# Optimization experiments

Hardware: AMD Instinct MI355X
Metric: run time of the kernel (lower is better)

## Reference

```python
import jax, jax.numpy as jnp
import numpy as np

GRID, BOXN, LABELN = 14, 2, 20
COORD_RATE, NOOBJ_RATE = 5.0, 0.5
CELL = 1.0 / GRID  # cell_size = 1/grid_num
ALL_BOX = 5 * BOXN


def setup_inputs() -> dict:
    key = jax.random.key(0)
    k1, k2, k3 = jax.random.split(key, 3)
    B = 4096
    C = ALL_BOX + LABELN  # 30
    preds = jax.random.uniform(k1, (B, GRID, GRID, C), dtype=jnp.float32)
    truths = jax.random.uniform(k2, (B, GRID, GRID, C), dtype=jnp.float32)
    objm = jax.random.uniform(k3, (B, GRID, GRID)) < 0.08
    truths = truths.at[..., 4].set(jnp.where(objm, truths[..., 4], 0.0))
    return {"preds": preds, "truths": truths}


def _yolo_loss(preds, truths):
    B = preds.shape[0]
    dt = preds.dtype
    obj = truths[..., 4] > 0                                   # [B,S,S]
    pb = preds[..., :ALL_BOX].reshape(*preds.shape[:3], BOXN, 5)  # [B,S,S,Bx,5]
    tb = truths[..., 0:4]                                       # [B,S,S,4]

    # ---- IoU of every predicted box vs the truth box of its cell ----
    pc = CELL * pb[..., 0:2]; ph = pb[..., 2:4] / 2.0
    tc = CELL * tb[..., 0:2]; th = tb[..., 2:4] / 2.0
    p_lt, p_rb = pc - ph, pc + ph                               # [B,S,S,Bx,2]
    t_lt, t_rb = (tc - th)[..., None, :], (tc + th)[..., None, :]  # [B,S,S,1,2]
    lt = jnp.maximum(p_lt, t_lt)
    rb = jnp.minimum(p_rb, t_rb)
    wh = jnp.clip(rb - lt, 0.0, None)
    inter = wh[..., 0] * wh[..., 1]                             # [B,S,S,Bx]
    pa = (p_rb[..., 0] - p_lt[..., 0]) * (p_rb[..., 1] - p_lt[..., 1])
    ta = (t_rb[..., 0] - t_lt[..., 0]) * (t_rb[..., 1] - t_lt[..., 1])
    ious = inter / (pa + ta - inter)                            # [B,S,S,Bx]

    # ---- responsible-box selection (argmax IoU; ties broken by max conf) ----
    max_iou = jnp.max(ious, axis=-1)                            # [B,S,S]
    tied = ious == max_iou[..., None]
    n_tied = tied.sum(-1)
    conf = pb[..., 4]                                           # [B,S,S,Bx]
    ind_conf = jnp.argmax(jnp.where(tied, conf, -jnp.inf), axis=-1)
    ind_iou = jnp.argmax(ious, axis=-1)
    resp = jnp.where(n_tied > 1, ind_conf, ind_iou)             # [B,S,S]
    resp_oh = jax.nn.one_hot(resp, BOXN, dtype=bool)            # [B,S,S,Bx]

    w_obj = obj.astype(dt)
    pred_resp = jnp.take_along_axis(pb, resp[..., None, None], axis=3)[..., 0, :]  # [B,S,S,5]
    tbox5 = truths[..., 0:5]

    center_loss = jnp.sum(w_obj[..., None] * (pred_resp[..., 0:2] - tbox5[..., 0:2]) ** 2)
    size_loss = jnp.sum(w_obj[..., None] * (jnp.sqrt(pred_resp[..., 2:4]) - jnp.sqrt(tbox5[..., 2:4])) ** 2)
    t_conf = jax.lax.stop_gradient(max_iou)  # .item() in torch detaches the IoU target
    conf_resp_loss = jnp.sum(w_obj * (pred_resp[..., 4] - t_conf) ** 2)
    noresp = (obj[..., None] & (~resp_oh)).astype(dt)
    conf_noresp_loss = jnp.sum(noresp * conf ** 2)
    conf_noobj_loss = jnp.sum((~obj)[..., None].astype(dt) * conf ** 2)
    label_loss = jnp.sum(w_obj[..., None] * (preds[..., ALL_BOX:] - truths[..., ALL_BOX:]) ** 2)

    return (COORD_RATE * (center_loss + size_loss) + conf_resp_loss
            + NOOBJ_RATE * conf_noresp_loss + NOOBJ_RATE * conf_noobj_loss
            + label_loss) / B


def reference(preds, truths):
    return _yolo_loss(preds, truths)
```

## Files before the change

kernel.cpp:

```cpp
#include <hip/hip_runtime.h>
#include <math.h>

#define GRIDN   14
#define BOXN    2
#define LABELN  20
#define ALL_BOX 10
#define CCH     30
#define CELLS_PER_BLOCK 256

__global__ void yolo_zero_kernel(float* out, int n) {
    int i = blockIdx.x * blockDim.x + threadIdx.x;
    if (i < n) out[i] = 0.0f;
}

__device__ __forceinline__ void async_load16(const float* g, float* l) {
    __builtin_amdgcn_global_load_lds(
        (const __attribute__((address_space(1))) void*)g,
        (__attribute__((address_space(3))) void*)l,
        16, 0, 0);
}

__global__ __launch_bounds__(256) void yolo_loss_kernel(
    const float* __restrict__ preds,
    const float* __restrict__ truths,
    float* __restrict__ out,
    int ncells)
{
#pragma clang fp contract(off)
    __shared__ float sP[CELLS_PER_BLOCK * CCH];
    __shared__ float sT[CELLS_PER_BLOCK * CCH];
    __shared__ float wsum[4];

    const int tid  = threadIdx.x;
    const int wave = tid >> 6;
    const int lane = tid & 63;
    const long long base = (long long)blockIdx.x * (CELLS_PER_BLOCK * CCH);

#pragma unroll
    for (int i = 0; i < 15; ++i) {
        const int c = wave + i * 4;
        const float* gsrc;
        float* ldst;
        if (c < 30) { gsrc = preds  + base + (long long)c * 256;        ldst = sP + c * 256; }
        else        { gsrc = truths + base + (long long)(c - 30) * 256; ldst = sT + (c - 30) * 256; }
        async_load16(gsrc + lane * 4, ldst);
    }
    __syncthreads();

    float cell_loss = 0.0f;
    const long long cell = (long long)blockIdx.x * CELLS_PER_BLOCK + tid;
    if (cell < ncells) {
        const float* p = sP + tid * CCH;
        const float* t = sT + tid * CCH;

        const float CELL = (float)(1.0 / (double)GRIDN);

        const float tx = t[0], ty = t[1], tw = t[2], th_ = t[3], tconf = t[4];
        const bool obj = tconf > 0.0f;

        const float tcx = CELL * tx, tcy = CELL * ty;
        const float thx = tw * 0.5f, thy = th_ * 0.5f;
        const float tltx = tcx - thx, tlty = tcy - thy;
        const float trbx = tcx + thx, trby = tcy + thy;
        const float ta = (trbx - tltx) * (trby - tlty);

        float iou[BOXN], conf[BOXN];
        float pr[BOXN][5];
#pragma unroll
        for (int b = 0; b < BOXN; ++b) {
            const float bx = p[b * 5 + 0], by = p[b * 5 + 1];
            const float bw = p[b * 5 + 2], bh = p[b * 5 + 3];
            const float bc = p[b * 5 + 4];
            pr[b][0] = bx; pr[b][1] = by; pr[b][2] = bw; pr[b][3] = bh; pr[b][4] = bc;
            conf[b] = bc;
            const float pcx = CELL * bx, pcy = CELL * by;
            const float phx = bw * 0.5f, phy = bh * 0.5f;
            const float pltx = pcx - phx, plty = pcy - phy;
            const float prbx = pcx + phx, prby = pcy + phy;
            const float ltx = fmaxf(pltx, tltx), lty = fmaxf(plty, tlty);
            const float rbx = fminf(prbx, trbx), rby = fminf(prby, trby);
            const float whx = fmaxf(rbx - ltx, 0.0f);
            const float why = fmaxf(rby - lty, 0.0f);
            const float inter = whx * why;
            const float pa = (prbx - pltx) * (prby - plty);
            iou[b] = inter / (pa + ta - inter);
        }

        const float max_iou = fmaxf(iou[0], iou[1]);
        int resp;
        if (iou[0] == iou[1]) resp = (conf[0] >= conf[1]) ? 0 : 1;
        else                  resp = (iou[0] > iou[1]) ? 0 : 1;

        const float* prr = pr[resp];

        const float dcx = prr[0] - tx;
        const float dcy = prr[1] - ty;
        const float center = dcx * dcx + dcy * dcy;

        const float dsx = sqrtf(prr[2]) - sqrtf(tw);
        const float dsy = sqrtf(prr[3]) - sqrtf(th_);
        const float size = dsx * dsx + dsy * dsy;

        const float dconf = prr[4] - max_iou;
        const float conf_resp = dconf * dconf;

        const float c_other = conf[1 - resp];
        const float conf_noresp = c_other * c_other;

        const float conf_noobj = conf[0] * conf[0] + conf[1] * conf[1];

        float label = 0.0f;
#pragma unroll
        for (int k = ALL_BOX; k < CCH; ++k) {
            const float d = p[k] - t[k];
            label += d * d;
        }

        const float w  = obj ? 1.0f : 0.0f;
        const float nw = obj ? 0.0f : 1.0f;
        cell_loss = w * (5.0f * (center + size) + conf_resp + 0.5f * conf_noresp + label)
                  + nw * (0.5f * conf_noobj);
    }

    float v = cell_loss;
#pragma unroll
    for (int off = 32; off > 0; off >>= 1) v += __shfl_down(v, off, 64);
    if (lane == 0) wsum[wave] = v;
    __syncthreads();
    if (tid == 0) {
        const float s = (wsum[0] + wsum[1]) + (wsum[2] + wsum[3]);
        atomicAdd(out, s * (1.0f / 4096.0f));
    }
}

extern "C" void kernel_launch(void* const* d_in, const int* in_sizes, int n_in,
                              void* d_out, int out_size, void* d_ws, size_t ws_size,
                              hipStream_t stream) {
    const float* preds  = (const float*)d_in[0];
    const float* truths = (const float*)d_in[1];
    float* out = (float*)d_out;

    const int ncells = in_sizes[0] / CCH;
    const int blocks = ncells / CELLS_PER_BLOCK;

    yolo_zero_kernel<<<(out_size + 255) / 256, 256, 0, stream>>>(out, out_size);
    yolo_loss_kernel<<<blocks, 256, 0, stream>>>(preds, truths, out, ncells);
}
```

Before: 206.4 us.

## Switch to persistent per-wave tiles with wave-local LDS staging

Replaces the one-block-per-256-cells launch with a fixed grid of 512 persistent blocks. Each wave independently loops over 64-cell tiles, stages them into its own LDS region with async global-to-LDS loads, and syncs with waitcnt instead of __syncthreads. It keeps a per-lane accumulator and does one atomic per wave at the end. This removes block-level barriers and per-block launch overhead, but each wave's load and compute for a tile run serially with no double buffering. It also issues more atomics (one per wave) and uses less LDS per wave, which may change occupancy and latency hiding.

```diff
diff --git a/kernel.cpp b/kernel.cpp
--- a/kernel.cpp
+++ b/kernel.cpp
@@ -6,7 +6,10 @@
 #define LABELN  20
 #define ALL_BOX 10
 #define CCH     30
-#define CELLS_PER_BLOCK 256
+#define TILE_CELLS  64
+#define TILE_FLOATS (TILE_CELLS * CCH)
+#define WAVES_PER_BLOCK 4
+#define PERSISTENT_BLOCKS 512
 
 __global__ void yolo_zero_kernel(float* out, int n) {
     int i = blockIdx.x * blockDim.x + threadIdx.x;
@@ -16,44 +19,57 @@
 __device__ __forceinline__ void async_load16(const float* g, float* l) {
     __builtin_amdgcn_global_load_lds(
         (const __attribute__((address_space(1))) void*)g,
-        (__attribute__((address_space(3))) void*)l,
-        16, 0, 0);
+        (__attribute__((address_space(3))) void*)l, 16, 0, 0);
 }
+__device__ __forceinline__ void async_load4(const float* g, float* l) {
+    __builtin_amdgcn_global_load_lds(
+        (const __attribute__((address_space(1))) void*)g,
+        (__attribute__((address_space(3))) void*)l, 4, 0, 0);
+}
+
+#define WAITCNT_VM0_ONLY   0x0F70
+#define WAITCNT_LGKM0_ONLY 0xC07F
 
 __global__ __launch_bounds__(256) void yolo_loss_kernel(
     const float* __restrict__ preds,
     const float* __restrict__ truths,
     float* __restrict__ out,
-    int ncells)
+    int ntiles)
 {
 #pragma clang fp contract(off)
-    __shared__ float sP[CELLS_PER_BLOCK * CCH];
-    __shared__ float sT[CELLS_PER_BLOCK * CCH];
-    __shared__ float wsum[4];
+    __shared__ float sbuf[WAVES_PER_BLOCK * 2 * TILE_FLOATS];
 
     const int tid  = threadIdx.x;
     const int wave = tid >> 6;
     const int lane = tid & 63;
-    const long long base = (long long)blockIdx.x * (CELLS_PER_BLOCK * CCH);
+
+    float* sP = sbuf + wave * (2 * TILE_FLOATS);
+    float* sT = sP + TILE_FLOATS;
+
+    const int gwave = blockIdx.x * WAVES_PER_BLOCK + wave;
+    const int nw    = gridDim.x * WAVES_PER_BLOCK;
+
+    const float CELL = (float)(1.0 / (double)GRIDN);
+    float acc = 0.0f;
+
+    for (int tile = gwave; tile < ntiles; tile += nw) {
+        const float* gp = preds  + (long long)tile * TILE_FLOATS;
+        const float* gt = truths + (long long)tile * TILE_FLOATS;
 
 #pragma unroll
-    for (int i = 0; i < 15; ++i) {
-        const int c = wave + i * 4;
-        const float* gsrc;
-        float* ldst;
-        if (c < 30) { gsrc = preds  + base + (long long)c * 256;        ldst = sP + c * 256; }
-        else        { gsrc = truths + base + (long long)(c - 30) * 256; ldst = sT + (c - 30) * 256; }
-        async_load16(gsrc + lane * 4, ldst);
-    }
-    __syncthreads();
+        for (int c = 0; c < 7; ++c) {
+            async_load16(gp + c * 256 + lane * 4, sP + c * 256);
+            async_load16(gt + c * 256 + lane * 4, sT + c * 256);
+        }
+#pragma unroll
+        for (int c = 0; c < 2; ++c) {
+            async_load4(gp + 1792 + c * 64 + lane, sP + 1792 + c * 64);
+            async_load4(gt + 1792 + c * 64 + lane, sT + 1792 + c * 64);
+        }
+        __builtin_amdgcn_s_waitcnt(WAITCNT_VM0_ONLY);
 
-    float cell_loss = 0.0f;
-    const long long cell = (long long)blockIdx.x * CELLS_PER_BLOCK + tid;
-    if (cell < ncells) {
-        const float* p = sP + tid * CCH;
-        const float* t = sT + tid * CCH;
-
-        const float CELL = (float)(1.0 / (double)GRIDN);
+        const float* p = sP + lane * CCH;
+        const float* t = sT + lane * CCH;
 
         const float tx = t[0], ty = t[1], tw = t[2], th_ = t[3], tconf = t[4];
         const bool obj = tconf > 0.0f;
@@ -117,20 +133,16 @@
         }
 
         const float w  = obj ? 1.0f : 0.0f;
-        const float nw = obj ? 0.0f : 1.0f;
-        cell_loss = w * (5.0f * (center + size) + conf_resp + 0.5f * conf_noresp + label)
-                  + nw * (0.5f * conf_noobj);
+        const float nw2 = obj ? 0.0f : 1.0f;
+        acc += w * (5.0f * (center + size) + conf_resp + 0.5f * conf_noresp + label)
+             + nw2 * (0.5f * conf_noobj);
+
+        __builtin_amdgcn_s_waitcnt(WAITCNT_LGKM0_ONLY);
     }
 
-    float v = cell_loss;
 #pragma unroll
-    for (int off = 32; off > 0; off >>= 1) v += __shfl_down(v, off, 64);
-    if (lane == 0) wsum[wave] = v;
-    __syncthreads();
-    if (tid == 0) {
-        const float s = (wsum[0] + wsum[1]) + (wsum[2] + wsum[3]);
-        atomicAdd(out, s * (1.0f / 4096.0f));
-    }
+    for (int off = 32; off > 0; off >>= 1) acc += __shfl_down(acc, off, 64);
+    if (lane == 0) atomicAdd(out, acc * (1.0f / 4096.0f));
 }
 
 extern "C" void kernel_launch(void* const* d_in, const int* in_sizes, int n_in,
@@ -141,8 +153,8 @@
     float* out = (float*)d_out;
 
     const int ncells = in_sizes[0] / CCH;
-    const int blocks = ncells / CELLS_PER_BLOCK;
+    const int ntiles = ncells / TILE_CELLS;
 
     yolo_zero_kernel<<<(out_size + 255) / 256, 256, 0, stream>>>(out, out_size);
-    yolo_loss_kernel<<<blocks, 256, 0, stream>>>(preds, truths, out, ncells);
+    yolo_loss_kernel<<<PERSISTENT_BLOCKS, 256, 0, stream>>>(preds, truths, out, ntiles);
 }
```

Result: no change. 209.0 us (+1.3%).

## Replace LDS staging with direct per-thread float2 global loads

Applied to the files above, without the earlier changes.

Drops the async global-to-LDS staging of 256 cells and the block barrier. Each thread now reads its own 30-float cell from preds and truths directly with float2 loads, skipping truth channels 5-9, which are never used. This removes about 61 KB of LDS per block, allowing more resident blocks (launch_bounds min 4), and cuts read traffic slightly. The cost is uncoalesced strided accesses, since consecutive lanes are 120 bytes apart, which depend on L1/L2 to merge.

```diff
diff --git a/kernel.cpp b/kernel.cpp
--- a/kernel.cpp
+++ b/kernel.cpp
@@ -6,56 +6,43 @@
 #define LABELN  20
 #define ALL_BOX 10
 #define CCH     30
-#define CELLS_PER_BLOCK 256
 
 __global__ void yolo_zero_kernel(float* out, int n) {
     int i = blockIdx.x * blockDim.x + threadIdx.x;
     if (i < n) out[i] = 0.0f;
 }
 
-__device__ __forceinline__ void async_load16(const float* g, float* l) {
-    __builtin_amdgcn_global_load_lds(
-        (const __attribute__((address_space(1))) void*)g,
-        (__attribute__((address_space(3))) void*)l,
-        16, 0, 0);
-}
-
-__global__ __launch_bounds__(256) void yolo_loss_kernel(
+__global__ __launch_bounds__(256, 4) void yolo_loss_kernel(
     const float* __restrict__ preds,
     const float* __restrict__ truths,
     float* __restrict__ out,
     int ncells)
 {
 #pragma clang fp contract(off)
-    __shared__ float sP[CELLS_PER_BLOCK * CCH];
-    __shared__ float sT[CELLS_PER_BLOCK * CCH];
     __shared__ float wsum[4];
 
     const int tid  = threadIdx.x;
     const int wave = tid >> 6;
     const int lane = tid & 63;
-    const long long base = (long long)blockIdx.x * (CELLS_PER_BLOCK * CCH);
 
-#pragma unroll
-    for (int i = 0; i < 15; ++i) {
-        const int c = wave + i * 4;
-        const float* gsrc;
-        float* ldst;
-        if (c < 30) { gsrc = preds  + base + (long long)c * 256;        ldst = sP + c * 256; }
-        else        { gsrc = truths + base + (long long)(c - 30) * 256; ldst = sT + (c - 30) * 256; }
-        async_load16(gsrc + lane * 4, ldst);
-    }
-    __syncthreads();
+    const long long cell = (long long)blockIdx.x * blockDim.x + tid;
 
     float cell_loss = 0.0f;
-    const long long cell = (long long)blockIdx.x * CELLS_PER_BLOCK + tid;
     if (cell < ncells) {
-        const float* p = sP + tid * CCH;
-        const float* t = sT + tid * CCH;
+        const float2* pp = (const float2*)(preds  + cell * CCH);
+        const float2* tp = (const float2*)(truths + cell * CCH);
+
+        float2 P[15];
+#pragma unroll
+        for (int i = 0; i < 15; ++i) P[i] = pp[i];
+        float2 T0 = tp[0], T1 = tp[1], T2 = tp[2];
+        float2 TL[10];
+#pragma unroll
+        for (int i = 0; i < 10; ++i) TL[i] = tp[5 + i];
 
         const float CELL = (float)(1.0 / (double)GRIDN);
 
-        const float tx = t[0], ty = t[1], tw = t[2], th_ = t[3], tconf = t[4];
+        const float tx = T0.x, ty = T0.y, tw = T1.x, th_ = T1.y, tconf = T2.x;
         const bool obj = tconf > 0.0f;
 
         const float tcx = CELL * tx, tcy = CELL * ty;
@@ -64,15 +51,16 @@
         const float trbx = tcx + thx, trby = tcy + thy;
         const float ta = (trbx - tltx) * (trby - tlty);
 
+        float pb[BOXN][5];
+        pb[0][0] = P[0].x; pb[0][1] = P[0].y; pb[0][2] = P[1].x; pb[0][3] = P[1].y; pb[0][4] = P[2].x;
+        pb[1][0] = P[2].y; pb[1][1] = P[3].x; pb[1][2] = P[3].y; pb[1][3] = P[4].x; pb[1][4] = P[4].y;
+
         float iou[BOXN], conf[BOXN];
-        float pr[BOXN][5];
 #pragma unroll
         for (int b = 0; b < BOXN; ++b) {
-            const float bx = p[b * 5 + 0], by = p[b * 5 + 1];
-            const float bw = p[b * 5 + 2], bh = p[b * 5 + 3];
-            const float bc = p[b * 5 + 4];
-            pr[b][0] = bx; pr[b][1] = by; pr[b][2] = bw; pr[b][3] = bh; pr[b][4] = bc;
-            conf[b] = bc;
+            const float bx = pb[b][0], by = pb[b][1];
+            const float bw = pb[b][2], bh = pb[b][3];
+            conf[b] = pb[b][4];
             const float pcx = CELL * bx, pcy = CELL * by;
             const float phx = bw * 0.5f, phy = bh * 0.5f;
             const float pltx = pcx - phx, plty = pcy - phy;
@@ -91,7 +79,7 @@
         if (iou[0] == iou[1]) resp = (conf[0] >= conf[1]) ? 0 : 1;
         else                  resp = (iou[0] > iou[1]) ? 0 : 1;
 
-        const float* prr = pr[resp];
+        const float* prr = pb[resp];
 
         const float dcx = prr[0] - tx;
         const float dcy = prr[1] - ty;
@@ -111,9 +99,11 @@
 
         float label = 0.0f;
 #pragma unroll
-        for (int k = ALL_BOX; k < CCH; ++k) {
-            const float d = p[k] - t[k];
-            label += d * d;
+        for (int i = 0; i < 10; ++i) {
+            const float dx = P[5 + i].x - TL[i].x;
+            label += dx * dx;
+            const float dy = P[5 + i].y - TL[i].y;
+            label += dy * dy;
         }
 
         const float w  = obj ? 1.0f : 0.0f;
@@ -141,7 +131,7 @@
     float* out = (float*)d_out;
 
     const int ncells = in_sizes[0] / CCH;
-    const int blocks = ncells / CELLS_PER_BLOCK;
+    const int blocks = (ncells + 255) / 256;
 
     yolo_zero_kernel<<<(out_size + 255) / 256, 256, 0, stream>>>(out, out_size);
     yolo_loss_kernel<<<blocks, 256, 0, stream>>>(preds, truths, out, ncells);
```

New measurement: 212.2 us. 1.03x slower.

## Replace LDS staging with direct per-thread vector loads of cell pairs

Applied to the files above, without the earlier changes.

Drops the global-to-LDS async staging and shared buffers. Each thread now processes two adjacent cells (60 floats, 16-byte aligned) using fifteen nontemporal float4 loads per tensor held in registers. This removes about 60KB of LDS per block, which limited occupancy, along with the barrier, and it halves the number of blocks. The cost is very high register use (120 floats per thread). Per-thread strided 240-byte loads are also poorly coalesced across a wave compared with the previous contiguous block loads.

```diff
diff --git a/kernel.cpp b/kernel.cpp
--- a/kernel.cpp
+++ b/kernel.cpp
@@ -6,123 +6,119 @@
 #define LABELN  20
 #define ALL_BOX 10
 #define CCH     30
-#define CELLS_PER_BLOCK 256
+
+typedef float vfloat4 __attribute__((ext_vector_type(4)));
 
 __global__ void yolo_zero_kernel(float* out, int n) {
     int i = blockIdx.x * blockDim.x + threadIdx.x;
     if (i < n) out[i] = 0.0f;
 }
 
-__device__ __forceinline__ void async_load16(const float* g, float* l) {
-    __builtin_amdgcn_global_load_lds(
-        (const __attribute__((address_space(1))) void*)g,
-        (__attribute__((address_space(3))) void*)l,
-        16, 0, 0);
+__device__ __forceinline__ float cell_loss(const float* p, const float* t) {
+#pragma clang fp contract(off)
+    const float CELL = (float)(1.0 / (double)GRIDN);
+
+    const float tx = t[0], ty = t[1], tw = t[2], th_ = t[3], tconf = t[4];
+    const bool obj = tconf > 0.0f;
+
+    const float tcx = CELL * tx, tcy = CELL * ty;
+    const float thx = tw * 0.5f, thy = th_ * 0.5f;
+    const float tltx = tcx - thx, tlty = tcy - thy;
+    const float trbx = tcx + thx, trby = tcy + thy;
+    const float ta = (trbx - tltx) * (trby - tlty);
+
+    float iou[BOXN], conf[BOXN];
+#pragma unroll
+    for (int b = 0; b < BOXN; ++b) {
+        const float bx = p[b * 5 + 0], by = p[b * 5 + 1];
+        const float bw = p[b * 5 + 2], bh = p[b * 5 + 3];
+        conf[b] = p[b * 5 + 4];
+        const float pcx = CELL * bx, pcy = CELL * by;
+        const float phx = bw * 0.5f, phy = bh * 0.5f;
+        const float pltx = pcx - phx, plty = pcy - phy;
+        const float prbx = pcx + phx, prby = pcy + phy;
+        const float ltx = fmaxf(pltx, tltx), lty = fmaxf(plty, tlty);
+        const float rbx = fminf(prbx, trbx), rby = fminf(prby, trby);
+        const float whx = fmaxf(rbx - ltx, 0.0f);
+        const float why = fmaxf(rby - lty, 0.0f);
+        const float inter = whx * why;
+        const float pa = (prbx - pltx) * (prby - plty);
+        iou[b] = inter / (pa + ta - inter);
+    }
+
+    const float max_iou = fmaxf(iou[0], iou[1]);
+    bool r1;
+    if (iou[0] == iou[1]) r1 = !(conf[0] >= conf[1]);
+    else                  r1 = !(iou[0] > iou[1]);
+
+    const float rx = r1 ? p[5] : p[0];
+    const float ry = r1 ? p[6] : p[1];
+    const float rw = r1 ? p[7] : p[2];
+    const float rh = r1 ? p[8] : p[3];
+    const float rc = r1 ? p[9] : p[4];
+
+    const float dcx = rx - tx;
+    const float dcy = ry - ty;
+    const float center = dcx * dcx + dcy * dcy;
+
+    const float dsx = sqrtf(rw) - sqrtf(tw);
+    const float dsy = sqrtf(rh) - sqrtf(th_);
+    const float size = dsx * dsx + dsy * dsy;
+
+    const float dconf = rc - max_iou;
+    const float conf_resp = dconf * dconf;
+
+    const float c_other = r1 ? conf[0] : conf[1];
+    const float conf_noresp = c_other * c_other;
+
+    const float conf_noobj = conf[0] * conf[0] + conf[1] * conf[1];
+
+    float label = 0.0f;
+#pragma unroll
+    for (int k = ALL_BOX; k < CCH; ++k) {
+        const float d = p[k] - t[k];
+        label += d * d;
+    }
+
+    const float w  = obj ? 1.0f : 0.0f;
+    const float nw = obj ? 0.0f : 1.0f;
+    return w * (5.0f * (center + size) + conf_resp + 0.5f * conf_noresp + label)
+         + nw * (0.5f * conf_noobj);
 }
 
-__global__ __launch_bounds__(256) void yolo_loss_kernel(
+__global__ __launch_bounds__(256, 2) void yolo_loss_kernel(
     const float* __restrict__ preds,
     const float* __restrict__ truths,
     float* __restrict__ out,
-    int ncells)
+    int npairs)
 {
 #pragma clang fp contract(off)
-    __shared__ float sP[CELLS_PER_BLOCK * CCH];
-    __shared__ float sT[CELLS_PER_BLOCK * CCH];
     __shared__ float wsum[4];
 
     const int tid  = threadIdx.x;
     const int wave = tid >> 6;
     const int lane = tid & 63;
-    const long long base = (long long)blockIdx.x * (CELLS_PER_BLOCK * CCH);
 
+    const long long pair = (long long)blockIdx.x * blockDim.x + tid;
+
+    float loss = 0.0f;
+    if (pair < npairs) {
+        const vfloat4* pp = (const vfloat4*)(preds  + pair * 60);
+        const vfloat4* tp = (const vfloat4*)(truths + pair * 60);
+
+        vfloat4 P4[15], T4[15];
 #pragma unroll
-    for (int i = 0; i < 15; ++i) {
-        const int c = wave + i * 4;
-        const float* gsrc;
-        float* ldst;
-        if (c < 30) { gsrc = preds  + base + (long long)c * 256;        ldst = sP + c * 256; }
-        else        { gsrc = truths + base + (long long)(c - 30) * 256; ldst = sT + (c - 30) * 256; }
-        async_load16(gsrc + lane * 4, ldst);
-    }
-    __syncthreads();
+        for (int i = 0; i < 15; ++i) P4[i] = __builtin_nontemporal_load(&pp[i]);
+#pragma unroll
+        for (int i = 0; i < 15; ++i) T4[i] = __builtin_nontemporal_load(&tp[i]);
+        __builtin_amdgcn_sched_barrier(0);
 
-    float cell_loss = 0.0f;
-    const long long cell = (long long)blockIdx.x * CELLS_PER_BLOCK + tid;
-    if (cell < ncells) {
-        const float* p = sP + tid * CCH;
-        const float* t = sT + tid * CCH;
-
-        const float CELL = (float)(1.0 / (double)GRIDN);
-
-        const float tx = t[0], ty = t[1], tw = t[2], th_ = t[3], tconf = t[4];
-        const bool obj = tconf > 0.0f;
-
-        const float tcx = CELL * tx, tcy = CELL * ty;
-        const float thx = tw * 0.5f, thy = th_ * 0.5f;
-        const float tltx = tcx - thx, tlty = tcy - thy;
-        const float trbx = tcx + thx, trby = tcy + thy;
-        const float ta = (trbx - tltx) * (trby - tlty);
-
-        float iou[BOXN], conf[BOXN];
-        float pr[BOXN][5];
-#pragma unroll
-        for (int b = 0; b < BOXN; ++b) {
-            const float bx = p[b * 5 + 0], by = p[b * 5 + 1];
-            const float bw = p[b * 5 + 2], bh = p[b * 5 + 3];
-            const float bc = p[b * 5 + 4];
-            pr[b][0] = bx; pr[b][1] = by; pr[b][2] = bw; pr[b][3] = bh; pr[b][4] = bc;
-            conf[b] = bc;
-            const float pcx = CELL * bx, pcy = CELL * by;
-            const float phx = bw * 0.5f, phy = bh * 0.5f;
-            const float pltx = pcx - phx, plty = pcy - phy;
-            const float prbx = pcx + phx, prby = pcy + phy;
-            const float ltx = fmaxf(pltx, tltx), lty = fmaxf(plty, tlty);
-            const float rbx = fminf(prbx, trbx), rby = fminf(prby, trby);
-            const float whx = fmaxf(rbx - ltx, 0.0f);
-            const float why = fmaxf(rby - lty, 0.0f);
-            const float inter = whx * why;
-            const float pa = (prbx - pltx) * (prby - plty);
-            iou[b] = inter / (pa + ta - inter);
-        }
-
-        const float max_iou = fmaxf(iou[0], iou[1]);
-        int resp;
-        if (iou[0] == iou[1]) resp = (conf[0] >= conf[1]) ? 0 : 1;
-        else                  resp = (iou[0] > iou[1]) ? 0 : 1;
-
-        const float* prr = pr[resp];
-
-        const float dcx = prr[0] - tx;
-        const float dcy = prr[1] - ty;
-        const float center = dcx * dcx + dcy * dcy;
-
-        const float dsx = sqrtf(prr[2]) - sqrtf(tw);
-        const float dsy = sqrtf(prr[3]) - sqrtf(th_);
-        const float size = dsx * dsx + dsy * dsy;
-
-        const float dconf = prr[4] - max_iou;
-        const float conf_resp = dconf * dconf;
-
-        const float c_other = conf[1 - resp];
-        const float conf_noresp = c_other * c_other;
-
-        const float conf_noobj = conf[0] * conf[0] + conf[1] * conf[1];
-
-        float label = 0.0f;
-#pragma unroll
-        for (int k = ALL_BOX; k < CCH; ++k) {
-            const float d = p[k] - t[k];
-            label += d * d;
-        }
-
-        const float w  = obj ? 1.0f : 0.0f;
-        const float nw = obj ? 0.0f : 1.0f;
-        cell_loss = w * (5.0f * (center + size) + conf_resp + 0.5f * conf_noresp + label)
-                  + nw * (0.5f * conf_noobj);
+        const float* P = (const float*)P4;
+        const float* T = (const float*)T4;
+        loss = cell_loss(P, T) + cell_loss(P + CCH, T + CCH);
     }
 
-    float v = cell_loss;
+    float v = loss;
 #pragma unroll
     for (int off = 32; off > 0; off >>= 1) v += __shfl_down(v, off, 64);
     if (lane == 0) wsum[wave] = v;
@@ -141,8 +137,9 @@
     float* out = (float*)d_out;
 
     const int ncells = in_sizes[0] / CCH;
-    const int blocks = ncells / CELLS_PER_BLOCK;
+    const int npairs = ncells / 2;
+    const int blocks = (npairs + 255) / 256;
 
     yolo_zero_kernel<<<(out_size + 255) / 256, 256, 0, stream>>>(out, out_size);
-    yolo_loss_kernel<<<blocks, 256, 0, stream>>>(preds, truths, out, ncells);
+    yolo_loss_kernel<<<blocks, 256, 0, stream>>>(preds, truths, out, npairs);
 }
```

Result: slower. 254.6 us (+23.4%).
